# Kernel optimization log

Measured on AMD Instinct MI355X. Metric: run time of the kernel, lower is better.

## Reference

```python
import jax, jax.numpy as jnp
import numpy as np

E = 16      # num_experts
H = 1024    # hidden_dim
I = 2048    # intermediate_dim
K = 2       # top_k routing
T = 2048    # tokens


def setup_inputs() -> dict:
    key = jax.random.key(0)
    k0, k1, k2, k3, k4 = jax.random.split(key, 5)
    std = 0.02  # nn.init.normal_(std=0.02) in _create_new_expert
    return {
        "x": jax.random.normal(k0, (T, H), dtype=jnp.float32),
        "w_router": jax.random.normal(k1, (H, E), dtype=jnp.float32) * std,
        "w_gate": jax.random.normal(k2, (E, H, I), dtype=jnp.float32) * std,
        "w_up": jax.random.normal(k3, (E, H, I), dtype=jnp.float32) * std,
        "w_down": jax.random.normal(k4, (E, I, H), dtype=jnp.float32) * std,
    }


def reference(x, w_router, w_gate, w_up, w_down):
    # --- router: softmax gating, top-k selection, renormalized weights ---
    logits = x @ w_router                                   # [T, E]
    probs = jax.nn.softmax(logits, axis=-1)                 # [T, E]
    vals, idx = jax.lax.top_k(probs, K)                     # [T, K]
    vals = vals / jnp.sum(vals, axis=-1, keepdims=True)     # renormalize over top-k
    # sparse combine weights: zero outside selected experts  [T, E]
    combine = jnp.sum(jax.nn.one_hot(idx, E, dtype=x.dtype) * vals[..., None], axis=1)
    # --- per-expert SwiGLU FFN (dense-over-experts, masked combine) ---
    gate = jnp.einsum('th,ehi->tei', x, w_gate)             # [T, E, I]
    up = jnp.einsum('th,ehi->tei', x, w_up)                 # [T, E, I]
    hidden = jax.nn.silu(gate) * up * combine[:, :, None]   # fuse combine weight
    y = jnp.einsum('tei,eih->th', hidden, w_down)           # [T, H]
    return y
```

## Files before the change

### kernel.cpp

```cpp
#include <hip/hip_runtime.h>
#include <hip/hip_bf16.h>
#include <math.h>


#define T_TOK 2048
#define H_DIM 1024
#define I_DIM 2048
#define E_NUM 16
#define N_ASSIGN 4096
#define BM 128
#define TILE_MAX 48

typedef __attribute__((ext_vector_type(8))) short short8;
typedef __attribute__((ext_vector_type(4))) float floatx4;

#define WS_OFF_COUNTS   0
#define WS_OFF_OFFSETS  64
#define WS_OFF_TOPKIDX  256
#define WS_OFF_TOPKW    (WS_OFF_TOPKIDX + 16384)
#define WS_OFF_ROWTOK   (WS_OFF_TOPKW  + 16384)
#define WS_OFF_ROWW     (WS_OFF_ROWTOK + 16384)
#define WS_OFF_TILEE    (WS_OFF_ROWW   + 16384)
#define WS_OFF_TILEM    (WS_OFF_TILEE  + 256)
#define WS_OFF_TILEC    (WS_OFF_TILEM  + 256)
#define WS_OFF_TOKROWS  (WS_OFF_TILEC  + 64)
#define WS_OFF_XG       (128 * 1024)
#define WS_OFF_H1       (WS_OFF_XG + 8u * 1024 * 1024)
#define WS_OFF_YP       (WS_OFF_H1 + 16u * 1024 * 1024)
#define WS_NEED_YP      42074112ull

__device__ __forceinline__ ushort f2bf(float f) {
    union { float f; unsigned int u; } v; v.f = f;
    unsigned int r = (v.u + 0x7fffu + ((v.u >> 16) & 1u)) >> 16;
    return (ushort)r;
}

__device__ __forceinline__ unsigned int cvt_pk_bf16(float lo, float hi) {
    unsigned int r;
    asm("v_cvt_pk_bf16_f32 %0, %1, %2" : "=v"(r) : "v"(lo), "v"(hi));
    return r;
}

#define FENCE_LGKM0() asm volatile("s_waitcnt lgkmcnt(0)" ::: "memory")
#define WAIT_VM(N)    asm volatile("s_waitcnt vmcnt(" #N ")" ::: "memory")
#define BARRIER_()                                    \
    do {                                              \
        FENCE_LGKM0();                                \
        __builtin_amdgcn_s_barrier();                 \
        asm volatile("" ::: "memory");                \
    } while (0)

__global__ __launch_bounds__(64)
void router_kernel(const float* __restrict__ x,
                   const float* __restrict__ wr,
                   int* __restrict__ counts,
                   int* __restrict__ topk_idx,
                   float* __restrict__ topk_w) {
    const int t = blockIdx.x;
    const int lane = threadIdx.x;
    const float* xt = x + (size_t)t * H_DIM;

    float acc[E_NUM];
#pragma unroll
    for (int e = 0; e < E_NUM; e++) acc[e] = 0.f;

    for (int h = lane; h < H_DIM; h += 64) {
        const float xv = xt[h];
        const float* wrow = wr + h * E_NUM;
#pragma unroll
        for (int e = 0; e < E_NUM; e++) acc[e] += xv * wrow[e];
    }
#pragma unroll
    for (int off = 32; off > 0; off >>= 1) {
#pragma unroll
        for (int e = 0; e < E_NUM; e++)
            acc[e] += __shfl_down(acc[e], off);
    }
    if (lane == 0) {
        int e0 = 0; float l0 = acc[0];
        for (int e = 1; e < E_NUM; e++)
            if (acc[e] > l0) { l0 = acc[e]; e0 = e; }
        int e1 = (e0 == 0) ? 1 : 0;
        float l1 = acc[e1];
        for (int e = 0; e < E_NUM; e++)
            if (e != e0 && acc[e] > l1) { l1 = acc[e]; e1 = e; }
        const float w0 = 1.f / (1.f + __expf(l1 - l0));
        const float w1 = 1.f - w0;
        topk_idx[t * 2 + 0] = e0;
        topk_idx[t * 2 + 1] = e1;
        topk_w[t * 2 + 0] = w0;
        topk_w[t * 2 + 1] = w1;
        atomicAdd(&counts[e0], 1);
        atomicAdd(&counts[e1], 1);
    }
}

__global__ __launch_bounds__(256)
void scatter_kernel(const int* __restrict__ counts,
                    int* __restrict__ offsets,
                    const int* __restrict__ topk_idx,
                    const float* __restrict__ topk_w,
                    int* __restrict__ row_token,
                    float* __restrict__ row_w,
                    int* __restrict__ tile_e,
                    int* __restrict__ tile_m,
                    int* __restrict__ tile_c,
                    int* __restrict__ token_rows) {
    __shared__ int base[E_NUM];
    __shared__ int fill[E_NUM];
    const int tid = threadIdx.x;
    if (tid == 0) {
        int run = 0, tc = 0;
        for (int e = 0; e < E_NUM; e++) {
            offsets[e] = run;
            base[e] = run;
            const int cnt = counts[e];
            run += cnt;
            for (int m = 0; m * BM < cnt; m++) {
                tile_e[tc] = e;
                tile_m[tc] = m;
                tc++;
            }
        }
        offsets[E_NUM] = run;
        *tile_c = tc;
    }
    if (tid < E_NUM) fill[tid] = 0;
    __syncthreads();
    for (int a = tid; a < N_ASSIGN; a += blockDim.x) {
        const int e = topk_idx[a];
        const int pos = atomicAdd(&fill[e], 1);
        const int dst = base[e] + pos;
        row_token[dst] = a >> 1;
        row_w[dst] = topk_w[a];
        token_rows[a] = dst;
    }
}

__global__ __launch_bounds__(256)
void gather_x_kernel(const float* __restrict__ x,
                     const int* __restrict__ row_token,
                     ushort* __restrict__ Xg) {
    const int r = blockIdx.x;
    const int t = row_token[r];
    const int c = threadIdx.x;
    floatx4 v = ((const floatx4*)(x + (size_t)t * H_DIM))[c];
    uint2 o;
    o.x = cvt_pk_bf16(v[0], v[1]);
    o.y = cvt_pk_bf16(v[2], v[3]);
    ((uint2*)(Xg + (size_t)r * H_DIM))[c] = o;
}

__global__ __launch_bounds__(256)
void gemm_gu_kernel(const ushort* __restrict__ Xg,
                    const float* __restrict__ wg,
                    const float* __restrict__ wu,
                    const int* __restrict__ offsets,
                    const float* __restrict__ row_w,
                    const int* __restrict__ tile_e,
                    const int* __restrict__ tile_m,
                    const int* __restrict__ tile_c,
                    ushort* __restrict__ h1) {
    if ((int)blockIdx.y >= *tile_c) return;
    const int e     = tile_e[blockIdx.y];
    const int mtile = tile_m[blockIdx.y];
    const int ntile = blockIdx.x;
    const int beg = offsets[e];
    const int n   = offsets[e + 1] - beg;

    __shared__ ushort As[2][BM * 32];
    __shared__ ushort Bgs[2][64 * 40];
    __shared__ ushort Bus[2][64 * 40];
    __shared__ float  wts[BM];

    const int tid  = threadIdx.x;
    const int lane = tid & 63;
    const int w    = tid >> 6;
    const int ml   = lane & 15;
    const int q    = lane >> 4;
    const int rq   = (ml >> 1) & 3;
    const int srcq = (lane & 3) ^ ((lane >> 3) & 3);

    if (tid < BM) {
        const int rl = mtile * BM + tid;
        wts[tid] = (rl < n) ? row_w[beg + rl] : 0.f;
    }

    floatx4 accg[2][4], accu[2][4];
#pragma unroll
    for (int i = 0; i < 2; i++)
#pragma unroll
        for (int j = 0; j < 4; j++) {
            accg[i][j] = (floatx4){0.f, 0.f, 0.f, 0.f};
            accu[i][j] = (floatx4){0.f, 0.f, 0.f, 0.f};
        }

    const ushort* Ap[2];
#pragma unroll
    for (int j = 0; j < 2; j++) {
        int row = beg + mtile * BM + 32 * w + 16 * j + (lane >> 2);
        row = row < 4095 ? row : 4095;
        Ap[j] = Xg + (size_t)row * H_DIM + srcq * 8;
    }

    const int kh = tid & 15;
    const int n4 = tid >> 4;
    const float* Bgp = wg + (size_t)e * H_DIM * I_DIM + ntile * 64 + n4 * 4;
    const float* Bup = wu + (size_t)e * H_DIM * I_DIM + ntile * 64 + n4 * 4;

    floatx4 g0p, g1p, u0p, u1p, g0q, g1q, u0q, u1q;

#define GU_ISSUE_A(k0v, buf)                                                   \
    {                                                                          \
        __builtin_amdgcn_global_load_lds(                                      \
            (const __attribute__((address_space(1))) unsigned int*)(Ap[0] + (k0v)), \
            (__attribute__((address_space(3))) unsigned int*)(&As[buf][(32 * w) * 32]), \
            16, 0, 0);                                                         \
        __builtin_amdgcn_global_load_lds(                                      \
            (const __attribute__((address_space(1))) unsigned int*)(Ap[1] + (k0v)), \
            (__attribute__((address_space(3))) unsigned int*)(&As[buf][(32 * w + 16) * 32]), \
            16, 0, 0);                                                         \
    }

#define GU_ISSUE_B(k0v, G0, G1, U0, U1)                                        \
    {                                                                          \
        const size_t boff = (size_t)((k0v) + 2 * kh) * I_DIM;                  \
        G0 = *(const floatx4*)(Bgp + boff);                                    \
        G1 = *(const floatx4*)(Bgp + boff + I_DIM);                            \
        U0 = *(const floatx4*)(Bup + boff);                                    \
        U1 = *(const floatx4*)(Bup + boff + I_DIM);                            \
    }

#define GU_CVT_B(buf, G0, G1, U0, U1)                                          \
    {                                                                          \
        _Pragma("unroll")                                                      \
        for (int j2 = 0; j2 < 4; j2++) {                                       \
            unsigned int pg = cvt_pk_bf16(G0[j2], G1[j2]);                     \
            unsigned int pu = cvt_pk_bf16(U0[j2], U1[j2]);                     \
            *(unsigned int*)&Bgs[buf][(n4 * 4 + j2) * 40 + 2 * kh] = pg;       \
            *(unsigned int*)&Bus[buf][(n4 * 4 + j2) * 40 + 2 * kh] = pu;       \
        }                                                                      \
    }

    GU_ISSUE_B(0, g0p, g1p, u0p, u1p);
    GU_ISSUE_A(0, 0);
    GU_ISSUE_B(32, g0q, g1q, u0q, u1q);
    GU_ISSUE_A(32, 1);
    WAIT_VM(6);
    GU_CVT_B(0, g0p, g1p, u0p, u1p);
    BARRIER_();

#define GU_STEP(cur, kpre, CG0, CG1, CU0, CU1, PG0, PG1, PU0, PU1)             \
    {                                                                          \
        short8 af[2], bgf[4], buf4[4];                                         \
        _Pragma("unroll")                                                      \
        for (int mt = 0; mt < 2; mt++)                                         \
            af[mt] = *(const short8*)&As[cur][(32 * w + mt * 16 + ml) * 32 +   \
                                              ((q ^ rq) * 8)];                 \
        FENCE_LGKM0();             \
        GU_ISSUE_B(kpre, PG0, PG1, PU0, PU1);                                  \
        GU_ISSUE_A(kpre, cur);                                                 \
        _Pragma("unroll")                                                      \
        for (int nt = 0; nt < 4; nt++) {                                       \
            bgf[nt]  = *(const short8*)&Bgs[cur][(nt * 16 + ml) * 40 + q * 8]; \
            buf4[nt] = *(const short8*)&Bus[cur][(nt * 16 + ml) * 40 + q * 8]; \
        }                                                                      \
        __builtin_amdgcn_s_setprio(1);                                         \
        _Pragma("unroll")                                                      \
        for (int mt = 0; mt < 2; mt++)                                         \
            _Pragma("unroll")                                                  \
            for (int nt = 0; nt < 4; nt++) {                                   \
                accg[mt][nt] = __builtin_amdgcn_mfma_f32_16x16x32_bf16(        \
                    af[mt], bgf[nt], accg[mt][nt], 0, 0, 0);                   \
                accu[mt][nt] = __builtin_amdgcn_mfma_f32_16x16x32_bf16(        \
                    af[mt], buf4[nt], accu[mt][nt], 0, 0, 0);                  \
            }                                                                  \
        __builtin_amdgcn_s_setprio(0);                                         \
        WAIT_VM(6);                                                            \
        GU_CVT_B(cur ^ 1, CG0, CG1, CU0, CU1);                                 \
        BARRIER_();                                                            \
    }

    for (int k0 = 0; k0 < H_DIM; k0 += 64) {
        const int kpe = (k0 + 64) & (H_DIM - 1);
        const int kpo = (k0 + 96) & (H_DIM - 1);
        GU_STEP(0, kpe, g0q, g1q, u0q, u1q, g0p, g1p, u0p, u1p);
        GU_STEP(1, kpo, g0p, g1p, u0p, u1p, g0q, g1q, u0q, u1q);
    }
#undef GU_STEP
#undef GU_CVT_B
#undef GU_ISSUE_B
#undef GU_ISSUE_A

#pragma unroll
    for (int mt = 0; mt < 2; mt++)
#pragma unroll
        for (int r = 0; r < 4; r++) {
            const int rloc = 32 * w + mt * 16 + q * 4 + r;
            const int rl = mtile * BM + rloc;
            if (rl < n) {
                const float cw = wts[rloc];
#pragma unroll
                for (int nt = 0; nt < 4; nt++) {
                    const float g = accg[mt][nt][r];
                    const float s = g / (1.f + __expf(-g));
                    h1[(size_t)(beg + rl) * I_DIM + ntile * 64 + nt * 16 + ml] =
                        f2bf(s * accu[mt][nt][r] * cw);
                }
            }
        }
}

template <int USE_YP>
__global__ __launch_bounds__(256)
void gemm_down_kernel(const ushort* __restrict__ h1,
                      const float* __restrict__ wd,
                      const int* __restrict__ offsets,
                      const int* __restrict__ row_token,
                      const int* __restrict__ tile_e,
                      const int* __restrict__ tile_m,
                      const int* __restrict__ tile_c,
                      float* __restrict__ y,
                      float* __restrict__ yp) {
    if ((int)blockIdx.y >= *tile_c) return;
    const int e     = tile_e[blockIdx.y];
    const int mtile = tile_m[blockIdx.y];
    const int ntile = blockIdx.x;
    const int kbase = USE_YP ? 0 : (int)blockIdx.z * 1024;
    const int KLEN  = USE_YP ? I_DIM : 1024;
    const int beg = offsets[e];
    const int n   = offsets[e + 1] - beg;

    __shared__ ushort As[2][BM * 32];
    __shared__ ushort Bs[2][64 * 40];
    __shared__ int    toks[BM];

    const int tid  = threadIdx.x;
    const int lane = tid & 63;
    const int w    = tid >> 6;
    const int ml   = lane & 15;
    const int q    = lane >> 4;
    const int rq   = (ml >> 1) & 3;
    const int srcq = (lane & 3) ^ ((lane >> 3) & 3);

    if (!USE_YP && tid < BM) {
        const int rl = mtile * BM + tid;
        toks[tid] = (rl < n) ? row_token[beg + rl] : 0;
    }

    floatx4 acc[2][4];
#pragma unroll
    for (int i = 0; i < 2; i++)
#pragma unroll
        for (int j = 0; j < 4; j++) acc[i][j] = (floatx4){0.f, 0.f, 0.f, 0.f};

    const ushort* Ap[2];
#pragma unroll
    for (int j = 0; j < 2; j++) {
        int row = beg + mtile * BM + 32 * w + 16 * j + (lane >> 2);
        row = row < 4095 ? row : 4095;
        Ap[j] = h1 + (size_t)row * I_DIM + kbase + srcq * 8;
    }

    const int kh = tid & 15;
    const int n4 = tid >> 4;
    const float* Bp = wd + (size_t)e * I_DIM * H_DIM +
                      (size_t)kbase * H_DIM + ntile * 64 + n4 * 4;

    floatx4 b0p, b1p, b0q, b1q;

#define D_ISSUE_A(k0v, buf)                                                    \
    {                                                                          \
        __builtin_amdgcn_global_load_lds(                                      \
            (const __attribute__((address_space(1))) unsigned int*)(Ap[0] + (k0v)), \
            (__attribute__((address_space(3))) unsigned int*)(&As[buf][(32 * w) * 32]), \
            16, 0, 0);                                                         \
        __builtin_amdgcn_global_load_lds(                                      \
            (const __attribute__((address_space(1))) unsigned int*)(Ap[1] + (k0v)), \
            (__attribute__((address_space(3))) unsigned int*)(&As[buf][(32 * w + 16) * 32]), \
            16, 0, 0);                                                         \
    }

#define D_ISSUE_B(k0v, B0, B1)                                                 \
    {                                                                          \
        const size_t boff = (size_t)((k0v) + 2 * kh) * H_DIM;                  \
        B0 = *(const floatx4*)(Bp + boff);                                     \
        B1 = *(const floatx4*)(Bp + boff + H_DIM);                             \
    }

#define D_CVT_B(buf, B0, B1)                                                   \
    {                                                                          \
        _Pragma("unroll")                                                      \
        for (int j2 = 0; j2 < 4; j2++) {                                       \
            unsigned int p = cvt_pk_bf16(B0[j2], B1[j2]);                      \
            *(unsigned int*)&Bs[buf][(n4 * 4 + j2) * 40 + 2 * kh] = p;         \
        }                                                                      \
    }

    D_ISSUE_B(0, b0p, b1p);
    D_ISSUE_A(0, 0);
    D_ISSUE_B(32, b0q, b1q);
    D_ISSUE_A(32, 1);
    WAIT_VM(4);
    D_CVT_B(0, b0p, b1p);
    BARRIER_();

#define D_STEP(cur, kpre, CB0, CB1, PB0, PB1)                                  \
    {                                                                          \
        short8 af[2], bfr[4];                                                  \
        _Pragma("unroll")                                                      \
        for (int mt = 0; mt < 2; mt++)                                         \
            af[mt] = *(const short8*)&As[cur][(32 * w + mt * 16 + ml) * 32 +   \
                                              ((q ^ rq) * 8)];                 \
        FENCE_LGKM0();                                                         \
        D_ISSUE_B(kpre, PB0, PB1);                                             \
        D_ISSUE_A(kpre, cur);                                                  \
        _Pragma("unroll")                                                      \
        for (int nt = 0; nt < 4; nt++)                                         \
            bfr[nt] = *(const short8*)&Bs[cur][(nt * 16 + ml) * 40 + q * 8];   \
        __builtin_amdgcn_s_setprio(1);                                         \
        _Pragma("unroll")                                                      \
        for (int mt = 0; mt < 2; mt++)                                         \
            _Pragma("unroll")                                                  \
            for (int nt = 0; nt < 4; nt++)                                     \
                acc[mt][nt] = __builtin_amdgcn_mfma_f32_16x16x32_bf16(         \
                    af[mt], bfr[nt], acc[mt][nt], 0, 0, 0);                    \
        __builtin_amdgcn_s_setprio(0);                                         \
        WAIT_VM(4);                                                            \
        D_CVT_B(cur ^ 1, CB0, CB1);                                            \
        BARRIER_();                                                            \
    }

    for (int k0 = 0; k0 < KLEN; k0 += 64) {
        const int kpe = (k0 + 64) & (KLEN - 1);
        const int kpo = (k0 + 96) & (KLEN - 1);
        D_STEP(0, kpe, b0q, b1q, b0p, b1p);
        D_STEP(1, kpo, b0p, b1p, b0q, b1q);
    }
#undef D_STEP
#undef D_CVT_B
#undef D_ISSUE_B
#undef D_ISSUE_A

#pragma unroll
    for (int mt = 0; mt < 2; mt++)
#pragma unroll
        for (int r = 0; r < 4; r++) {
            const int rloc = 32 * w + mt * 16 + q * 4 + r;
            const int rl = mtile * BM + rloc;
            if (rl < n) {
                if (USE_YP) {
#pragma unroll
                    for (int nt = 0; nt < 4; nt++)
                        yp[(size_t)(beg + rl) * H_DIM + ntile * 64 + nt * 16 + ml] =
                            acc[mt][nt][r];
                } else {
                    const int t = toks[rloc];
#pragma unroll
                    for (int nt = 0; nt < 4; nt++)
                        atomicAdd(&y[(size_t)t * H_DIM + ntile * 64 + nt * 16 + ml],
                                  acc[mt][nt][r]);
                }
            }
        }
}

__global__ __launch_bounds__(256)
void combine_kernel(const float* __restrict__ yp,
                    const int* __restrict__ token_rows,
                    float* __restrict__ y) {
    const int t = blockIdx.x;
    const int c = threadIdx.x;
    const int r0 = token_rows[2 * t];
    const int r1 = token_rows[2 * t + 1];
    floatx4 a = ((const floatx4*)(yp + (size_t)r0 * H_DIM))[c];
    floatx4 b = ((const floatx4*)(yp + (size_t)r1 * H_DIM))[c];
    ((floatx4*)(y + (size_t)t * H_DIM))[c] = a + b;
}

extern "C" void kernel_launch(void* const* d_in, const int* in_sizes, int n_in,
                              void* d_out, int out_size, void* d_ws, size_t ws_size,
                              hipStream_t stream) {
    const float* x  = (const float*)d_in[0];
    const float* wr = (const float*)d_in[1];
    const float* wg = (const float*)d_in[2];
    const float* wu = (const float*)d_in[3];
    const float* wd = (const float*)d_in[4];
    float* y = (float*)d_out;

    char* ws = (char*)d_ws;
    int*    counts    = (int*)(ws + WS_OFF_COUNTS);
    int*    offsets   = (int*)(ws + WS_OFF_OFFSETS);
    int*    topk_idx  = (int*)(ws + WS_OFF_TOPKIDX);
    float*  topk_w    = (float*)(ws + WS_OFF_TOPKW);
    int*    row_token = (int*)(ws + WS_OFF_ROWTOK);
    float*  row_w     = (float*)(ws + WS_OFF_ROWW);
    int*    tile_e    = (int*)(ws + WS_OFF_TILEE);
    int*    tile_m    = (int*)(ws + WS_OFF_TILEM);
    int*    tile_c    = (int*)(ws + WS_OFF_TILEC);
    int*    token_rows= (int*)(ws + WS_OFF_TOKROWS);
    ushort* Xg        = (ushort*)(ws + WS_OFF_XG);
    ushort* h1        = (ushort*)(ws + WS_OFF_H1);
    float*  yp        = (float*)(ws + WS_OFF_YP);

    const bool use_yp = ws_size >= WS_NEED_YP;

    hipMemsetAsync(counts, 0, 64, stream);
    if (!use_yp)
        hipMemsetAsync(y, 0, (size_t)T_TOK * H_DIM * sizeof(float), stream);

    router_kernel<<<T_TOK, 64, 0, stream>>>(x, wr, counts, topk_idx, topk_w);
    scatter_kernel<<<1, 256, 0, stream>>>(counts, offsets, topk_idx, topk_w,
                                          row_token, row_w, tile_e, tile_m, tile_c,
                                          token_rows);
    gather_x_kernel<<<N_ASSIGN, 256, 0, stream>>>(x, row_token, Xg);
    gemm_gu_kernel<<<dim3(I_DIM / 64, TILE_MAX), 256, 0, stream>>>(
        Xg, wg, wu, offsets, row_w, tile_e, tile_m, tile_c, h1);
    if (use_yp) {
        gemm_down_kernel<1><<<dim3(H_DIM / 64, TILE_MAX), 256, 0, stream>>>(
            h1, wd, offsets, row_token, tile_e, tile_m, tile_c, y, yp);
        combine_kernel<<<T_TOK, 256, 0, stream>>>(yp, token_rows, y);
    } else {
        gemm_down_kernel<0><<<dim3(H_DIM / 64, TILE_MAX, 2), 256, 0, stream>>>(
            h1, wd, offsets, row_token, tile_e, tile_m, tile_c, y, yp);
    }
}
```

Before: 581.3 us.

## Pre-transpose expert weights to bf16 and use direct-to-LDS bf16 GEMMs

Adds a transpose-and-convert kernel that rewrites the gate, up and down expert weights into K-contiguous bf16 copies in workspace on every call. New gate/up and down GEMM kernels then stream both operands with global_load_lds, which removes the per-tile fp32 register loads and in-loop bf16 conversion. The cost is an extra full read of the fp32 weights and a bf16 write each call, plus three more launches. The new path only runs if the workspace holds about 243 MB, and otherwise falls back to the old kernels.

```diff
diff --git a/kernel.cpp b/kernel.cpp
--- a/kernel.cpp
+++ b/kernel.cpp
@@ -28,6 +28,10 @@
 #define WS_OFF_H1       (WS_OFF_XG + 8u * 1024 * 1024)
 #define WS_OFF_YP       (WS_OFF_H1 + 16u * 1024 * 1024)
 #define WS_NEED_YP      42074112ull
+#define WS_OFF_WGT      (WS_OFF_YP + 16u * 1024 * 1024)
+#define WS_OFF_WUT      (WS_OFF_WGT + 64u * 1024 * 1024)
+#define WS_OFF_WDT      (WS_OFF_WUT + 64u * 1024 * 1024)
+#define WS_NEED_BF16    243400704ull
 
 __device__ __forceinline__ ushort f2bf(float f) {
     union { float f; unsigned int u; } v; v.f = f;
@@ -49,6 +53,9 @@
         __builtin_amdgcn_s_barrier();                 \
         asm volatile("" ::: "memory");                \
     } while (0)
+
+typedef const __attribute__((address_space(1))) unsigned int* gas_p;
+typedef __attribute__((address_space(3))) unsigned int* las_p;
 
 __global__ __launch_bounds__(64)
 void router_kernel(const float* __restrict__ x,
@@ -152,6 +159,270 @@
 }
 
 __global__ __launch_bounds__(256)
+void transpose_cvt_kernel(const float* __restrict__ in,
+                          ushort* __restrict__ out,
+                          int R, int C) {
+    __shared__ float tile[64][65];
+    const int z  = blockIdx.z;
+    const int r0 = blockIdx.y * 64;
+    const int c0 = blockIdx.x * 64;
+    const int tid = threadIdx.x;
+    const float* src = in + ((size_t)z * R + r0) * C + c0;
+    const int rx = tid & 15;
+    const int ry = tid >> 4;
+#pragma unroll
+    for (int p = 0; p < 4; p++) {
+        const int r = ry * 4 + p;
+        floatx4 v = *(const floatx4*)(src + (size_t)r * C + rx * 4);
+#pragma unroll
+        for (int j = 0; j < 4; j++) tile[rx * 4 + j][r] = v[j];
+    }
+    __syncthreads();
+    const int cx = tid & 7;
+    const int cy = tid >> 3;
+    ushort* dst = out + ((size_t)z * C + c0) * R + r0;
+#pragma unroll
+    for (int p = 0; p < 2; p++) {
+        const int c = cy + p * 32;
+        uint4 o;
+        o.x = cvt_pk_bf16(tile[c][cx * 8 + 0], tile[c][cx * 8 + 1]);
+        o.y = cvt_pk_bf16(tile[c][cx * 8 + 2], tile[c][cx * 8 + 3]);
+        o.z = cvt_pk_bf16(tile[c][cx * 8 + 4], tile[c][cx * 8 + 5]);
+        o.w = cvt_pk_bf16(tile[c][cx * 8 + 6], tile[c][cx * 8 + 7]);
+        *(uint4*)(dst + (size_t)c * R + cx * 8) = o;
+    }
+}
+
+__global__ __launch_bounds__(256)
+void gemm_gu_bf16_kernel(const ushort* __restrict__ Xg,
+                         const ushort* __restrict__ wgT,
+                         const ushort* __restrict__ wuT,
+                         const int* __restrict__ offsets,
+                         const float* __restrict__ row_w,
+                         const int* __restrict__ tile_e,
+                         const int* __restrict__ tile_m,
+                         const int* __restrict__ tile_c,
+                         ushort* __restrict__ h1) {
+    if ((int)blockIdx.y >= *tile_c) return;
+    const int e     = tile_e[blockIdx.y];
+    const int mtile = tile_m[blockIdx.y];
+    const int ntile = blockIdx.x;
+    const int beg = offsets[e];
+    const int n   = offsets[e + 1] - beg;
+
+    __shared__ ushort As[2][BM * 32];
+    __shared__ ushort Bgs[2][64 * 32];
+    __shared__ ushort Bus[2][64 * 32];
+    __shared__ float  wts[BM];
+
+    const int tid  = threadIdx.x;
+    const int lane = tid & 63;
+    const int w    = tid >> 6;
+    const int ml   = lane & 15;
+    const int q    = lane >> 4;
+    const int rq   = (ml >> 1) & 3;
+    const int srcq = (lane & 3) ^ ((lane >> 3) & 3);
+
+    if (tid < BM) {
+        const int rl = mtile * BM + tid;
+        wts[tid] = (rl < n) ? row_w[beg + rl] : 0.f;
+    }
+
+    floatx4 accg[2][4], accu[2][4];
+#pragma unroll
+    for (int i = 0; i < 2; i++)
+#pragma unroll
+        for (int j = 0; j < 4; j++) {
+            accg[i][j] = (floatx4){0.f, 0.f, 0.f, 0.f};
+            accu[i][j] = (floatx4){0.f, 0.f, 0.f, 0.f};
+        }
+
+    const ushort* Ap[2];
+#pragma unroll
+    for (int j = 0; j < 2; j++) {
+        int row = beg + mtile * BM + 32 * w + 16 * j + (lane >> 2);
+        row = row < 4095 ? row : 4095;
+        Ap[j] = Xg + (size_t)row * H_DIM + srcq * 8;
+    }
+    const int brow = ntile * 64 + 16 * w + (lane >> 2);
+    const ushort* Bgp = wgT + ((size_t)e * I_DIM + brow) * H_DIM + srcq * 8;
+    const ushort* Bup = wuT + ((size_t)e * I_DIM + brow) * H_DIM + srcq * 8;
+
+#define GU2_STAGE(buf, k0v)                                                    \
+    {                                                                          \
+        __builtin_amdgcn_global_load_lds((gas_p)(Ap[0] + (k0v)),               \
+            (las_p)(&As[buf][(32 * w) * 32]), 16, 0, 0);                       \
+        __builtin_amdgcn_global_load_lds((gas_p)(Ap[1] + (k0v)),               \
+            (las_p)(&As[buf][(32 * w + 16) * 32]), 16, 0, 0);                  \
+        __builtin_amdgcn_global_load_lds((gas_p)(Bgp + (k0v)),                 \
+            (las_p)(&Bgs[buf][(16 * w) * 32]), 16, 0, 0);                      \
+        __builtin_amdgcn_global_load_lds((gas_p)(Bup + (k0v)),                 \
+            (las_p)(&Bus[buf][(16 * w) * 32]), 16, 0, 0);                      \
+    }
+
+#define GU2_STEP(cur, kpre, dopre)                                             \
+    {                                                                          \
+        if (dopre) GU2_STAGE(cur ^ 1, kpre);                                   \
+        short8 af[2], bg[4], bu[4];                                            \
+        _Pragma("unroll")                                                      \
+        for (int mt = 0; mt < 2; mt++)                                         \
+            af[mt] = *(const short8*)&As[cur][(32 * w + mt * 16 + ml) * 32 +   \
+                                              ((q ^ rq) * 8)];                 \
+        _Pragma("unroll")                                                      \
+        for (int nt = 0; nt < 4; nt++) {                                       \
+            bg[nt] = *(const short8*)&Bgs[cur][(nt * 16 + ml) * 32 +           \
+                                              ((q ^ rq) * 8)];                 \
+            bu[nt] = *(const short8*)&Bus[cur][(nt * 16 + ml) * 32 +           \
+                                              ((q ^ rq) * 8)];                 \
+        }                                                                      \
+        __builtin_amdgcn_s_setprio(1);                                         \
+        _Pragma("unroll")                                                      \
+        for (int mt = 0; mt < 2; mt++)                                         \
+            _Pragma("unroll")                                                  \
+            for (int nt = 0; nt < 4; nt++) {                                   \
+                accg[mt][nt] = __builtin_amdgcn_mfma_f32_16x16x32_bf16(        \
+                    af[mt], bg[nt], accg[mt][nt], 0, 0, 0);                    \
+                accu[mt][nt] = __builtin_amdgcn_mfma_f32_16x16x32_bf16(        \
+                    af[mt], bu[nt], accu[mt][nt], 0, 0, 0);                    \
+            }                                                                  \
+        __builtin_amdgcn_s_setprio(0);                                         \
+        WAIT_VM(0);                                                            \
+        BARRIER_();                                                            \
+    }
+
+    GU2_STAGE(0, 0);
+    WAIT_VM(0);
+    BARRIER_();
+
+    for (int k0 = 0; k0 < H_DIM; k0 += 64) {
+        GU2_STEP(0, k0 + 32, 1);
+        GU2_STEP(1, k0 + 64, (k0 + 64 < H_DIM));
+    }
+#undef GU2_STEP
+#undef GU2_STAGE
+
+#pragma unroll
+    for (int mt = 0; mt < 2; mt++)
+#pragma unroll
+        for (int r = 0; r < 4; r++) {
+            const int rloc = 32 * w + mt * 16 + q * 4 + r;
+            const int rl = mtile * BM + rloc;
+            if (rl < n) {
+                const float cw = wts[rloc];
+#pragma unroll
+                for (int nt = 0; nt < 4; nt++) {
+                    const float g = accg[mt][nt][r];
+                    const float s = g / (1.f + __expf(-g));
+                    h1[(size_t)(beg + rl) * I_DIM + ntile * 64 + nt * 16 + ml] =
+                        f2bf(s * accu[mt][nt][r] * cw);
+                }
+            }
+        }
+}
+
+__global__ __launch_bounds__(256)
+void gemm_down_bf16_kernel(const ushort* __restrict__ h1,
+                           const ushort* __restrict__ wdT,
+                           const int* __restrict__ offsets,
+                           const int* __restrict__ tile_e,
+                           const int* __restrict__ tile_m,
+                           const int* __restrict__ tile_c,
+                           float* __restrict__ yp) {
+    if ((int)blockIdx.y >= *tile_c) return;
+    const int e     = tile_e[blockIdx.y];
+    const int mtile = tile_m[blockIdx.y];
+    const int ntile = blockIdx.x;
+    const int beg = offsets[e];
+    const int n   = offsets[e + 1] - beg;
+
+    __shared__ ushort As[2][BM * 32];
+    __shared__ ushort Bs[2][64 * 32];
+
+    const int tid  = threadIdx.x;
+    const int lane = tid & 63;
+    const int w    = tid >> 6;
+    const int ml   = lane & 15;
+    const int q    = lane >> 4;
+    const int rq   = (ml >> 1) & 3;
+    const int srcq = (lane & 3) ^ ((lane >> 3) & 3);
+
+    floatx4 acc[2][4];
+#pragma unroll
+    for (int i = 0; i < 2; i++)
+#pragma unroll
+        for (int j = 0; j < 4; j++) acc[i][j] = (floatx4){0.f, 0.f, 0.f, 0.f};
+
+    const ushort* Ap[2];
+#pragma unroll
+    for (int j = 0; j < 2; j++) {
+        int row = beg + mtile * BM + 32 * w + 16 * j + (lane >> 2);
+        row = row < 4095 ? row : 4095;
+        Ap[j] = h1 + (size_t)row * I_DIM + srcq * 8;
+    }
+    const int brow = ntile * 64 + 16 * w + (lane >> 2);
+    const ushort* Bp = wdT + ((size_t)e * H_DIM + brow) * I_DIM + srcq * 8;
+
+#define D2_STAGE(buf, k0v)                                                     \
+    {                                                                          \
+        __builtin_amdgcn_global_load_lds((gas_p)(Ap[0] + (k0v)),               \
+            (las_p)(&As[buf][(32 * w) * 32]), 16, 0, 0);                       \
+        __builtin_amdgcn_global_load_lds((gas_p)(Ap[1] + (k0v)),               \
+            (las_p)(&As[buf][(32 * w + 16) * 32]), 16, 0, 0);                  \
+        __builtin_amdgcn_global_load_lds((gas_p)(Bp + (k0v)),                  \
+            (las_p)(&Bs[buf][(16 * w) * 32]), 16, 0, 0);                       \
+    }
+
+#define D2_STEP(cur, kpre, dopre)                                              \
+    {                                                                          \
+        if (dopre) D2_STAGE(cur ^ 1, kpre);                                    \
+        short8 af[2], bfr[4];                                                  \
+        _Pragma("unroll")                                                      \
+        for (int mt = 0; mt < 2; mt++)                                         \
+            af[mt] = *(const short8*)&As[cur][(32 * w + mt * 16 + ml) * 32 +   \
+                                              ((q ^ rq) * 8)];                 \
+        _Pragma("unroll")                                                      \
+        for (int nt = 0; nt < 4; nt++)                                         \
+            bfr[nt] = *(const short8*)&Bs[cur][(nt * 16 + ml) * 32 +           \
+                                              ((q ^ rq) * 8)];                 \
+        __builtin_amdgcn_s_setprio(1);                                         \
+        _Pragma("unroll")                                                      \
+        for (int mt = 0; mt < 2; mt++)                                         \
+            _Pragma("unroll")                                                  \
+            for (int nt = 0; nt < 4; nt++)                                     \
+                acc[mt][nt] = __builtin_amdgcn_mfma_f32_16x16x32_bf16(         \
+                    af[mt], bfr[nt], acc[mt][nt], 0, 0, 0);                    \
+        __builtin_amdgcn_s_setprio(0);                                         \
+        WAIT_VM(0);                                                            \
+        BARRIER_();                                                            \
+    }
+
+    D2_STAGE(0, 0);
+    WAIT_VM(0);
+    BARRIER_();
+
+    for (int k0 = 0; k0 < I_DIM; k0 += 64) {
+        D2_STEP(0, k0 + 32, 1);
+        D2_STEP(1, k0 + 64, (k0 + 64 < I_DIM));
+    }
+#undef D2_STEP
+#undef D2_STAGE
+
+#pragma unroll
+    for (int mt = 0; mt < 2; mt++)
+#pragma unroll
+        for (int r = 0; r < 4; r++) {
+            const int rloc = 32 * w + mt * 16 + q * 4 + r;
+            const int rl = mtile * BM + rloc;
+            if (rl < n) {
+#pragma unroll
+                for (int nt = 0; nt < 4; nt++)
+                    yp[(size_t)(beg + rl) * H_DIM + ntile * 64 + nt * 16 + ml] =
+                        acc[mt][nt][r];
+            }
+        }
+}
+
+__global__ __launch_bounds__(256)
 void gemm_gu_kernel(const ushort* __restrict__ Xg,
                     const float* __restrict__ wg,
                     const float* __restrict__ wu,
@@ -212,14 +483,10 @@
 
 #define GU_ISSUE_A(k0v, buf)                                                   \
     {                                                                          \
-        __builtin_amdgcn_global_load_lds(                                      \
-            (const __attribute__((address_space(1))) unsigned int*)(Ap[0] + (k0v)), \
-            (__attribute__((address_space(3))) unsigned int*)(&As[buf][(32 * w) * 32]), \
-            16, 0, 0);                                                         \
-        __builtin_amdgcn_global_load_lds(                                      \
-            (const __attribute__((address_space(1))) unsigned int*)(Ap[1] + (k0v)), \
-            (__attribute__((address_space(3))) unsigned int*)(&As[buf][(32 * w + 16) * 32]), \
-            16, 0, 0);                                                         \
+        __builtin_amdgcn_global_load_lds((gas_p)(Ap[0] + (k0v)),               \
+            (las_p)(&As[buf][(32 * w) * 32]), 16, 0, 0);                       \
+        __builtin_amdgcn_global_load_lds((gas_p)(Ap[1] + (k0v)),               \
+            (las_p)(&As[buf][(32 * w + 16) * 32]), 16, 0, 0);                  \
     }
 
 #define GU_ISSUE_B(k0v, G0, G1, U0, U1)                                        \
@@ -257,7 +524,7 @@
         for (int mt = 0; mt < 2; mt++)                                         \
             af[mt] = *(const short8*)&As[cur][(32 * w + mt * 16 + ml) * 32 +   \
                                               ((q ^ rq) * 8)];                 \
-        FENCE_LGKM0();             \
+        FENCE_LGKM0();                                                         \
         GU_ISSUE_B(kpre, PG0, PG1, PU0, PU1);                                  \
         GU_ISSUE_A(kpre, cur);                                                 \
         _Pragma("unroll")                                                      \
@@ -371,14 +638,10 @@
 
 #define D_ISSUE_A(k0v, buf)                                                    \
     {                                                                          \
-        __builtin_amdgcn_global_load_lds(                                      \
-            (const __attribute__((address_space(1))) unsigned int*)(Ap[0] + (k0v)), \
-            (__attribute__((address_space(3))) unsigned int*)(&As[buf][(32 * w) * 32]), \
-            16, 0, 0);                                                         \
-        __builtin_amdgcn_global_load_lds(                                      \
-            (const __attribute__((address_space(1))) unsigned int*)(Ap[1] + (k0v)), \
-            (__attribute__((address_space(3))) unsigned int*)(&As[buf][(32 * w + 16) * 32]), \
-            16, 0, 0);                                                         \
+        __builtin_amdgcn_global_load_lds((gas_p)(Ap[0] + (k0v)),               \
+            (las_p)(&As[buf][(32 * w) * 32]), 16, 0, 0);                       \
+        __builtin_amdgcn_global_load_lds((gas_p)(Ap[1] + (k0v)),               \
+            (las_p)(&As[buf][(32 * w + 16) * 32]), 16, 0, 0);                  \
     }
 
 #define D_ISSUE_B(k0v, B0, B1)                                                 \
@@ -502,8 +765,12 @@
     ushort* Xg        = (ushort*)(ws + WS_OFF_XG);
     ushort* h1        = (ushort*)(ws + WS_OFF_H1);
     float*  yp        = (float*)(ws + WS_OFF_YP);
-
-    const bool use_yp = ws_size >= WS_NEED_YP;
+    ushort* wgT       = (ushort*)(ws + WS_OFF_WGT);
+    ushort* wuT       = (ushort*)(ws + WS_OFF_WUT);
+    ushort* wdT       = (ushort*)(ws + WS_OFF_WDT);
+
+    const bool use_bf16w = ws_size >= WS_NEED_BF16;
+    const bool use_yp    = ws_size >= WS_NEED_YP;
 
     hipMemsetAsync(counts, 0, 64, stream);
     if (!use_yp)
@@ -514,13 +781,28 @@
                                           row_token, row_w, tile_e, tile_m, tile_c,
                                           token_rows);
     gather_x_kernel<<<N_ASSIGN, 256, 0, stream>>>(x, row_token, Xg);
-    gemm_gu_kernel<<<dim3(I_DIM / 64, TILE_MAX), 256, 0, stream>>>(
-        Xg, wg, wu, offsets, row_w, tile_e, tile_m, tile_c, h1);
-    if (use_yp) {
+
+    if (use_bf16w) {
+        transpose_cvt_kernel<<<dim3(I_DIM / 64, H_DIM / 64, E_NUM), 256, 0, stream>>>(
+            wg, wgT, H_DIM, I_DIM);
+        transpose_cvt_kernel<<<dim3(I_DIM / 64, H_DIM / 64, E_NUM), 256, 0, stream>>>(
+            wu, wuT, H_DIM, I_DIM);
+        transpose_cvt_kernel<<<dim3(H_DIM / 64, I_DIM / 64, E_NUM), 256, 0, stream>>>(
+            wd, wdT, I_DIM, H_DIM);
+        gemm_gu_bf16_kernel<<<dim3(I_DIM / 64, TILE_MAX), 256, 0, stream>>>(
+            Xg, wgT, wuT, offsets, row_w, tile_e, tile_m, tile_c, h1);
+        gemm_down_bf16_kernel<<<dim3(H_DIM / 64, TILE_MAX), 256, 0, stream>>>(
+            h1, wdT, offsets, tile_e, tile_m, tile_c, yp);
+        combine_kernel<<<T_TOK, 256, 0, stream>>>(yp, token_rows, y);
+    } else if (use_yp) {
+        gemm_gu_kernel<<<dim3(I_DIM / 64, TILE_MAX), 256, 0, stream>>>(
+            Xg, wg, wu, offsets, row_w, tile_e, tile_m, tile_c, h1);
         gemm_down_kernel<1><<<dim3(H_DIM / 64, TILE_MAX), 256, 0, stream>>>(
             h1, wd, offsets, row_token, tile_e, tile_m, tile_c, y, yp);
         combine_kernel<<<T_TOK, 256, 0, stream>>>(yp, token_rows, y);
     } else {
+        gemm_gu_kernel<<<dim3(I_DIM / 64, TILE_MAX), 256, 0, stream>>>(
+            Xg, wg, wu, offsets, row_w, tile_e, tile_m, tile_c, h1);
         gemm_down_kernel<0><<<dim3(H_DIM / 64, TILE_MAX, 2), 256, 0, stream>>>(
             h1, wd, offsets, row_token, tile_e, tile_m, tile_c, y, yp);
     }
```

Result: slower. 618.4 us (+6.4%).
